# Optimization experiments

Measured on AMD Instinct MI355X. Metric: run time of the kernel, lower is better.

## Reference

```python
import jax, jax.numpy as jnp
import numpy as np

B, F, T, EPT, S, E, H, LVL = 16384, 512, 4, 2, 2, 256, 128, 2

def _ple_level(xs_task, x_sh, w_task, b_task, w_sh, b_sh, w_gate, b_gate, w_gsh=None, b_gsh=None):
    # xs_task: [T,B,I] per-task inputs; x_sh: [B,I] shared input
    task_out = jax.nn.relu(jnp.einsum('tbi,teio->tbeo', xs_task, w_task) + b_task[:, None])  # [T,B,EPT,E]
    sh_out = jax.nn.relu(jnp.einsum('bi,sio->bso', x_sh, w_sh) + b_sh)                       # [B,S,E]
    t = task_out.shape[0]
    experts = jnp.concatenate([task_out, jnp.broadcast_to(sh_out[None], (t,) + sh_out.shape)], axis=2)  # [T,B,EPT+S,E]
    gate = jax.nn.softmax(jnp.einsum('tbi,tig->tbg', xs_task, w_gate) + b_gate[:, None], axis=-1)
    task_next = jnp.einsum('tbg,tbge->tbe', gate, experts)  # [T,B,E]
    sh_next = None
    if w_gsh is not None:
        # all experts ordered task0_exp0, task0_exp1, task1_exp0, ..., then shared
        bsz = x_sh.shape[0]
        all_exp = jnp.concatenate([jnp.transpose(task_out, (1, 0, 2, 3)).reshape(bsz, -1, task_out.shape[-1]), sh_out], axis=1)
        gsh = jax.nn.softmax(x_sh @ w_gsh + b_gsh, axis=-1)
        sh_next = jnp.einsum('bg,bge->be', gsh, all_exp)
    return task_next, sh_next

def setup_inputs() -> dict:
    key = jax.random.key(0)
    ks = jax.random.split(key, 16)
    sc = 0.02
    d = {
        'x': jax.random.normal(ks[0], (B, F), jnp.float32),
        # level 0 (in_dim=F, has shared gate)
        'w_task0': jax.random.normal(ks[1], (T, EPT, F, E), jnp.float32) * sc,
        'b_task0': jnp.zeros((T, EPT, E), jnp.float32),
        'w_sh0': jax.random.normal(ks[2], (S, F, E), jnp.float32) * sc,
        'b_sh0': jnp.zeros((S, E), jnp.float32),
        'w_gate0': jax.random.normal(ks[3], (T, F, EPT + S), jnp.float32) * sc,
        'b_gate0': jnp.zeros((T, EPT + S), jnp.float32),
        'w_gsh0': jax.random.normal(ks[4], (F, T * EPT + S), jnp.float32) * sc,
        'b_gsh0': jnp.zeros((T * EPT + S,), jnp.float32),
        # level 1 (last; in_dim=E, no shared gate)
        'w_task1': jax.random.normal(ks[5], (T, EPT, E, E), jnp.float32) * sc,
        'b_task1': jnp.zeros((T, EPT, E), jnp.float32),
        'w_sh1': jax.random.normal(ks[6], (S, E, E), jnp.float32) * sc,
        'b_sh1': jnp.zeros((S, E), jnp.float32),
        'w_gate1': jax.random.normal(ks[7], (T, E, EPT + S), jnp.float32) * sc,
        'b_gate1': jnp.zeros((T, EPT + S), jnp.float32),
        # towers
        'w_tw': jax.random.normal(ks[8], (T, E, H), jnp.float32) * sc,
        'b_tw': jnp.zeros((T, H), jnp.float32),
        'w_out': jax.random.normal(ks[9], (T, H, 2), jnp.float32) * sc,
        'b_out': jnp.zeros((T, 2), jnp.float32),
    }
    return d

def reference(x, w_task0, b_task0, w_sh0, b_sh0, w_gate0, b_gate0, w_gsh0, b_gsh0,
              w_task1, b_task1, w_sh1, b_sh1, w_gate1, b_gate1,
              w_tw, b_tw, w_out, b_out):
    xs_task = jnp.broadcast_to(x[None], (T,) + x.shape)  # all tasks see same input at level 0
    t1, sh1 = _ple_level(xs_task, x, w_task0, b_task0, w_sh0, b_sh0, w_gate0, b_gate0, w_gsh0, b_gsh0)
    t2, _ = _ple_level(t1, sh1, w_task1, b_task1, w_sh1, b_sh1, w_gate1, b_gate1)
    h = jax.nn.relu(jnp.einsum('tbe,teh->tbh', t2, w_tw) + b_tw[:, None])
    logits = jnp.einsum('tbh,tho->tbo', h, w_out) + b_out[:, None]
    p = jax.nn.softmax(logits, axis=-1)
    return jnp.clip(p, 1e-15, 1.0 - 1e-15)  # [T,B,2]
```

## Files before the change

kernel.cpp:

```cpp
#include <hip/hip_runtime.h>

typedef unsigned short u16;
typedef __bf16 bf16x8 __attribute__((ext_vector_type(8)));
typedef float f32x4 __attribute__((ext_vector_type(4)));
typedef u16 u16x8 __attribute__((ext_vector_type(8)));

#define B_ 16384

__device__ __forceinline__ u16 f2b(float f){
  unsigned u = __builtin_bit_cast(unsigned, f);
  u = (u + 0x7FFFu + ((u >> 16) & 1u)) >> 16;
  return (u16)u;
}
__device__ __forceinline__ float b2f(u16 v){
  return __builtin_bit_cast(float, ((unsigned)v) << 16);
}
__device__ __forceinline__ void ld8(const u16* __restrict__ p, float* f){
  u16x8 v = *(const u16x8*)p;
  #pragma unroll
  for (int j = 0; j < 8; ++j) f[j] = b2f(v[j]);
}
__device__ __forceinline__ void st8(u16* __restrict__ p, const float* f){
  u16x8 v;
  #pragma unroll
  for (int j = 0; j < 8; ++j) v[j] = f2b(f[j]);
  *(u16x8*)p = v;
}

__device__ __forceinline__ void gload16(const u16* g, u16* lds){
  __builtin_amdgcn_global_load_lds(
      (const __attribute__((address_space(1))) unsigned int*)g,
      (__attribute__((address_space(3))) unsigned int*)lds, 16, 0, 0);
}

__device__ __forceinline__ void gemm_core4(const u16* __restrict__ A,
                                           const u16* __restrict__ Wt,
                                           int K, int m0, int n0, int nt,
                                           u16* sm, f32x4 acc[4][4])
{
  const int tid  = threadIdx.x;
  const int lane = tid & 63;
  const int wave = tid >> 6;
  const int wm   = ((tid >> 7) & 1) * 64;
  const int wn   = ((tid >> 6) & 1) * 64;

  f32x4 zero = {0.f, 0.f, 0.f, 0.f};
  #pragma unroll
  for (int mi = 0; mi < 4; ++mi)
    #pragma unroll
    for (int ni = 0; ni < 4; ++ni) acc[mi][ni] = zero;

  const int srow  = lane >> 3;
  const int gslot = (lane & 7) ^ srow;
  const u16* gsrc[8];
  int gdst[8];
  #pragma unroll
  for (int i = 0; i < 8; ++i) {
    int c = wave * 8 + i;
    if (c < 16) {
      gsrc[i] = A + (size_t)(m0 + c * 8 + srow) * K + gslot * 8;
      gdst[i] = c * 512;
    } else {
      gsrc[i] = Wt + (size_t)(n0 + (c - 16) * 8 + srow) * K + gslot * 8;
      gdst[i] = 8192 + (c - 16) * 512;
    }
  }

  int aoff[2][4], boff[2][4];
  #pragma unroll
  for (int kk = 0; kk < 2; ++kk) {
    #pragma unroll
    for (int m = 0; m < 4; ++m) {
      int r = wm + m * 16 + (lane & 15);
      aoff[kk][m] = r * 64 + (((kk * 4 + (lane >> 4)) ^ (r & 7)) * 8);
    }
    #pragma unroll
    for (int n = 0; n < 4; ++n) {
      int r = wn + n * 16 + (lane & 15);
      boff[kk][n] = 8192 + r * 64 + (((kk * 4 + (lane >> 4)) ^ (r & 7)) * 8);
    }
  }

  #pragma unroll
  for (int i = 0; i < 8; ++i) gload16(gsrc[i], sm + gdst[i]);
  asm volatile("s_waitcnt vmcnt(0)" ::: "memory");
  __builtin_amdgcn_s_barrier();

  for (int j = 0; j < nt; ++j) {
    if (j + 1 < nt) {
      u16* base = sm + ((j + 1) & 1) * 16384;
      #pragma unroll
      for (int i = 0; i < 8; ++i) gload16(gsrc[i] + (size_t)(j + 1) * 64, base + gdst[i]);
    }
    const u16* sa = sm + (j & 1) * 16384;
    #pragma unroll
    for (int kk = 0; kk < 2; ++kk) {
      bf16x8 av[4], bv[4];
      #pragma unroll
      for (int m = 0; m < 4; ++m) av[m] = *(const bf16x8*)(sa + aoff[kk][m]);
      #pragma unroll
      for (int n = 0; n < 4; ++n) bv[n] = *(const bf16x8*)(sa + boff[kk][n]);
      #pragma unroll
      for (int m = 0; m < 4; ++m)
        #pragma unroll
        for (int n = 0; n < 4; ++n)
          acc[m][n] = __builtin_amdgcn_mfma_f32_16x16x32_bf16(av[m], bv[n], acc[m][n], 0, 0, 0);
    }
    if (j + 1 < nt) {
      asm volatile("s_waitcnt vmcnt(0)" ::: "memory");
      __builtin_amdgcn_s_barrier();
    }
  }
}


__global__ __launch_bounds__(256) void k_gemm0(const u16* __restrict__ xb,
    const u16* __restrict__ Wt0, const float* __restrict__ bias0,
    u16* __restrict__ E0, float* __restrict__ G0L)
{
  __shared__ __align__(16) u16 sm[32768];
  f32x4 acc[4][4];
  const int bid = blockIdx.x;
  const int swz = (bid & 7) * 336 + (bid >> 3);
  const int m0 = (swz / 21) * 128, n0 = (swz % 21) * 128;
  gemm_core4(xb, Wt0, 512, m0, n0, 8, sm, acc);
  const int lane = threadIdx.x & 63;
  const int wm = ((threadIdx.x >> 7) & 1) * 64, wn = ((threadIdx.x >> 6) & 1) * 64;
  #pragma unroll
  for (int mi = 0; mi < 4; ++mi)
    #pragma unroll
    for (int ni = 0; ni < 4; ++ni) {
      int gcol = n0 + wn + ni * 16 + (lane & 15);
      float bias = bias0[gcol];
      #pragma unroll
      for (int r = 0; r < 4; ++r) {
        int grow = m0 + wm + mi * 16 + ((lane >> 4) << 2) + r;
        float v = acc[mi][ni][r] + bias;
        if (gcol < 2560)      E0[(size_t)grow * 2560 + gcol] = f2b(fmaxf(v, 0.f));
        else if (gcol < 2586) G0L[(size_t)grow * 26 + (gcol - 2560)] = v;
      }
    }
}

__global__ __launch_bounds__(256) void k_mix0(const u16* __restrict__ E0,
    const float* __restrict__ G0L, u16* __restrict__ T1SH)
{
  const int b = blockIdx.x * 8 + (threadIdx.x >> 5);
  const int e0 = (threadIdx.x & 31) * 8;
  const float* gl = G0L + (size_t)b * 26;
  float g[4][4];
  #pragma unroll
  for (int t = 0; t < 4; ++t) {
    float l0 = gl[t*4+0], l1 = gl[t*4+1], l2 = gl[t*4+2], l3 = gl[t*4+3];
    float m = fmaxf(fmaxf(l0, l1), fmaxf(l2, l3));
    float e0e = expf(l0-m), e1 = expf(l1-m), e2 = expf(l2-m), e3 = expf(l3-m);
    float inv = 1.f / (e0e + e1 + e2 + e3);
    g[t][0] = e0e*inv; g[t][1] = e1*inv; g[t][2] = e2*inv; g[t][3] = e3*inv;
  }
  float gs[10];
  {
    float m = gl[16];
    #pragma unroll
    for (int j = 1; j < 10; ++j) m = fmaxf(m, gl[16 + j]);
    float s = 0.f;
    #pragma unroll
    for (int j = 0; j < 10; ++j) { gs[j] = expf(gl[16 + j] - m); s += gs[j]; }
    float inv = 1.f / s;
    #pragma unroll
    for (int j = 0; j < 10; ++j) gs[j] *= inv;
  }
  const u16* row = E0 + (size_t)b * 2560;
  float sh0[8], sh1[8], shacc[8];
  ld8(row + 2048 + e0, sh0);
  ld8(row + 2304 + e0, sh1);
  #pragma unroll
  for (int j = 0; j < 8; ++j) shacc[j] = gs[8]*sh0[j] + gs[9]*sh1[j];
  #pragma unroll
  for (int t = 0; t < 4; ++t) {
    float te0[8], te1[8], v[8];
    ld8(row + (t*2+0)*256 + e0, te0);
    ld8(row + (t*2+1)*256 + e0, te1);
    #pragma unroll
    for (int j = 0; j < 8; ++j) {
      v[j] = g[t][0]*te0[j] + g[t][1]*te1[j] + g[t][2]*sh0[j] + g[t][3]*sh1[j];
      shacc[j] += gs[t*2+0]*te0[j] + gs[t*2+1]*te1[j];
    }
    st8(T1SH + ((size_t)t * B_ + b) * 256 + e0, v);
  }
  st8(T1SH + ((size_t)4 * B_ + b) * 256 + e0, shacc);
}

__global__ __launch_bounds__(256) void k_gemm1(const u16* __restrict__ T1SH,
    const u16* __restrict__ Wt1, const float* __restrict__ bias1,
    u16* __restrict__ E1, float* __restrict__ G1L, u16* __restrict__ SH1E)
{
  const int z = blockIdx.z;
  const int m0 = blockIdx.x * 128, n0 = blockIdx.y * 128;
  if (z == 4 && n0 >= 512) return;
  __shared__ __align__(16) u16 sm[32768];
  f32x4 acc[4][4];
  gemm_core4(T1SH + (size_t)z * B_ * 256, Wt1 + (size_t)z * 640 * 256, 256, m0, n0, 4, sm, acc);
  const int lane = threadIdx.x & 63;
  const int wm = ((threadIdx.x >> 7) & 1) * 64, wn = ((threadIdx.x >> 6) & 1) * 64;
  const float* bias = bias1 + z * 640;
  #pragma unroll
  for (int mi = 0; mi < 4; ++mi)
    #pragma unroll
    for (int ni = 0; ni < 4; ++ni) {
      int gcol = n0 + wn + ni * 16 + (lane & 15);
      float bv = bias[gcol];
      #pragma unroll
      for (int r = 0; r < 4; ++r) {
        int grow = m0 + wm + mi * 16 + ((lane >> 4) << 2) + r;
        float v = acc[mi][ni][r] + bv;
        if (z < 4) {
          if (gcol < 512)      E1[((size_t)z * B_ + grow) * 512 + gcol] = f2b(fmaxf(v, 0.f));
          else if (gcol < 516) G1L[((size_t)z * B_ + grow) * 4 + (gcol - 512)] = v;
        } else {
          if (gcol < 512)      SH1E[(size_t)grow * 512 + gcol] = f2b(fmaxf(v, 0.f));
        }
      }
    }
}

__global__ __launch_bounds__(256) void k_mix1(const u16* __restrict__ E1,
    const float* __restrict__ G1L, const u16* __restrict__ SH1E, u16* __restrict__ T2)
{
  const int b = blockIdx.x * 8 + (threadIdx.x >> 5);
  const int e0 = (threadIdx.x & 31) * 8;
  float sh0[8], sh1[8];
  ld8(SH1E + (size_t)b * 512 + e0, sh0);
  ld8(SH1E + (size_t)b * 512 + 256 + e0, sh1);
  #pragma unroll
  for (int t = 0; t < 4; ++t) {
    const float* gl = G1L + ((size_t)t * B_ + b) * 4;
    float l0 = gl[0], l1 = gl[1], l2 = gl[2], l3 = gl[3];
    float m = fmaxf(fmaxf(l0, l1), fmaxf(l2, l3));
    float x0 = expf(l0-m), x1 = expf(l1-m), x2 = expf(l2-m), x3 = expf(l3-m);
    float inv = 1.f / (x0 + x1 + x2 + x3);
    float g0 = x0*inv, g1 = x1*inv, g2 = x2*inv, g3 = x3*inv;
    float te0[8], te1[8], v[8];
    ld8(E1 + ((size_t)t * B_ + b) * 512 + e0, te0);
    ld8(E1 + ((size_t)t * B_ + b) * 512 + 256 + e0, te1);
    #pragma unroll
    for (int j = 0; j < 8; ++j)
      v[j] = g0*te0[j] + g1*te1[j] + g2*sh0[j] + g3*sh1[j];
    st8(T2 + ((size_t)t * B_ + b) * 256 + e0, v);
  }
}

__global__ __launch_bounds__(256) void k_tower(const u16* __restrict__ T2,
    const u16* __restrict__ Wtw, const float* __restrict__ b_tw,
    const float* __restrict__ w_out, const float* __restrict__ b_out,
    float* __restrict__ out)
{
  __shared__ __align__(16) u16 sm[32768];
  __shared__ float part[2][128][2];
  f32x4 acc[4][4];
  const int z = blockIdx.z;
  const int m0 = blockIdx.x * 128;
  gemm_core4(T2 + (size_t)z * B_ * 256, Wtw + (size_t)z * 128 * 256, 256, m0, 0, 4, sm, acc);
  const int lane = threadIdx.x & 63;
  const int wm = ((threadIdx.x >> 7) & 1) * 64, wn = ((threadIdx.x >> 6) & 1) * 64;
  #pragma unroll
  for (int mi = 0; mi < 4; ++mi) {
    #pragma unroll
    for (int r = 0; r < 4; ++r) {
      float p0 = 0.f, p1 = 0.f;
      #pragma unroll
      for (int ni = 0; ni < 4; ++ni) {
        int col = wn + ni * 16 + (lane & 15);
        float h = fmaxf(acc[mi][ni][r] + b_tw[z * 128 + col], 0.f);
        p0 += h * w_out[(z * 128 + col) * 2 + 0];
        p1 += h * w_out[(z * 128 + col) * 2 + 1];
      }
      #pragma unroll
      for (int off = 1; off < 16; off <<= 1) {
        p0 += __shfl_xor(p0, off);
        p1 += __shfl_xor(p1, off);
      }
      if ((lane & 15) == 0) {
        int rowl = wm + mi * 16 + ((lane >> 4) << 2) + r;
        part[wn >> 6][rowl][0] = p0;
        part[wn >> 6][rowl][1] = p1;
      }
    }
  }
  __syncthreads();
  if (threadIdx.x < 128) {
    int rowl = threadIdx.x;
    float l0 = part[0][rowl][0] + part[1][rowl][0] + b_out[z * 2 + 0];
    float l1 = part[0][rowl][1] + part[1][rowl][1] + b_out[z * 2 + 1];
    float mx = fmaxf(l0, l1);
    float e0 = expf(l0 - mx), e1 = expf(l1 - mx);
    float inv = 1.f / (e0 + e1);
    float p0 = fminf(fmaxf(e0 * inv, 1e-15f), 1.0f);
    float p1 = fminf(fmaxf(e1 * inv, 1e-15f), 1.0f);
    size_t o = ((size_t)z * B_ + m0 + rowl) * 2;
    out[o] = p0; out[o + 1] = p1;
  }
}

__global__ void k_prep(const float* __restrict__ x,
    const float* __restrict__ w_task0, const float* __restrict__ b_task0,
    const float* __restrict__ w_sh0,   const float* __restrict__ b_sh0,
    const float* __restrict__ w_gate0, const float* __restrict__ b_gate0,
    const float* __restrict__ w_gsh0,  const float* __restrict__ b_gsh0,
    const float* __restrict__ w_task1, const float* __restrict__ b_task1,
    const float* __restrict__ w_sh1,   const float* __restrict__ b_sh1,
    const float* __restrict__ w_gate1, const float* __restrict__ b_gate1,
    const float* __restrict__ w_tw,
    u16* __restrict__ xb, u16* __restrict__ Wt0, float* __restrict__ bias0,
    u16* __restrict__ Wt1, float* __restrict__ bias1, u16* __restrict__ Wtw)
{
  size_t i = (size_t)blockIdx.x * 256 + threadIdx.x;
  const size_t S_X8  = (size_t)16384 * 512 / 8;
  const size_t S_WT0 = (size_t)2688 * 512;
  const size_t S_B0  = 2688;
  const size_t S_WT1 = (size_t)5 * 640 * 256;
  const size_t S_B1  = 5 * 640;
  const size_t S_WTW = (size_t)4 * 128 * 256;

  if (i < S_X8) {
    size_t o = i * 8;
    float4 a = *(const float4*)(x + o);
    float4 b = *(const float4*)(x + o + 4);
    u16x8 v;
    v[0] = f2b(a.x); v[1] = f2b(a.y); v[2] = f2b(a.z); v[3] = f2b(a.w);
    v[4] = f2b(b.x); v[5] = f2b(b.y); v[6] = f2b(b.z); v[7] = f2b(b.w);
    *(u16x8*)(xb + o) = v;
    return;
  }
  i -= S_X8;
  if (i < S_WT0) {
    int c = (int)(i / 512), f = (int)(i % 512);
    float v = 0.f;
    if (c < 2048)      { int te = c >> 8, o = c & 255; v = w_task0[((size_t)te * 512 + f) * 256 + o]; }
    else if (c < 2560) { int s = (c - 2048) >> 8, o = c & 255; v = w_sh0[((size_t)s * 512 + f) * 256 + o]; }
    else if (c < 2576) { int q = c - 2560; int t = q >> 2, gg = q & 3; v = w_gate0[((size_t)t * 512 + f) * 4 + gg]; }
    else if (c < 2586) { int j = c - 2576; v = w_gsh0[(size_t)f * 10 + j]; }
    Wt0[i] = f2b(v);
    return;
  }
  i -= S_WT0;
  if (i < S_B0) {
    int c = (int)i; float v = 0.f;
    if (c < 2048)      { int te = c >> 8, o = c & 255; v = b_task0[te * 256 + o]; }
    else if (c < 2560) { int s = (c - 2048) >> 8, o = c & 255; v = b_sh0[s * 256 + o]; }
    else if (c < 2576) { v = b_gate0[c - 2560]; }
    else if (c < 2586) { v = b_gsh0[c - 2576]; }
    bias0[c] = v;
    return;
  }
  i -= S_B0;
  if (i < S_WT1) {
    int z = (int)(i / (640 * 256)); int rem = (int)(i % (640 * 256));
    int c = rem / 256, f = rem % 256;
    float v = 0.f;
    if (z < 4) {
      if (c < 512)      { int ee = c >> 8, o = c & 255; v = w_task1[(((size_t)(z * 2 + ee)) * 256 + f) * 256 + o]; }
      else if (c < 516) { int gg = c - 512; v = w_gate1[((size_t)z * 256 + f) * 4 + gg]; }
    } else {
      if (c < 512)      { int s = c >> 8, o = c & 255; v = w_sh1[((size_t)s * 256 + f) * 256 + o]; }
    }
    Wt1[i] = f2b(v);
    return;
  }
  i -= S_WT1;
  if (i < S_B1) {
    int z = (int)(i / 640); int c = (int)(i % 640);
    float v = 0.f;
    if (z < 4) {
      if (c < 512)      { int ee = c >> 8, o = c & 255; v = b_task1[(z * 2 + ee) * 256 + o]; }
      else if (c < 516) { v = b_gate1[z * 4 + (c - 512)]; }
    } else {
      if (c < 512)      { int s = c >> 8, o = c & 255; v = b_sh1[s * 256 + o]; }
    }
    bias1[(size_t)z * 640 + c] = v;
    return;
  }
  i -= S_B1;
  if (i < S_WTW) {
    int z = (int)(i / (128 * 256)); int rem = (int)(i % (128 * 256));
    int h = rem / 256, f = rem % 256;
    Wtw[i] = f2b(w_tw[((size_t)z * 256 + f) * 128 + h]);
    return;
  }
}

extern "C" void kernel_launch(void* const* d_in, const int* in_sizes, int n_in,
                              void* d_out, int out_size, void* d_ws, size_t ws_size,
                              hipStream_t stream)
{
  (void)in_sizes; (void)n_in; (void)out_size; (void)ws_size;
  const float* x       = (const float*)d_in[0];
  const float* w_task0 = (const float*)d_in[1];
  const float* b_task0 = (const float*)d_in[2];
  const float* w_sh0   = (const float*)d_in[3];
  const float* b_sh0   = (const float*)d_in[4];
  const float* w_gate0 = (const float*)d_in[5];
  const float* b_gate0 = (const float*)d_in[6];
  const float* w_gsh0  = (const float*)d_in[7];
  const float* b_gsh0  = (const float*)d_in[8];
  const float* w_task1 = (const float*)d_in[9];
  const float* b_task1 = (const float*)d_in[10];
  const float* w_sh1   = (const float*)d_in[11];
  const float* b_sh1   = (const float*)d_in[12];
  const float* w_gate1 = (const float*)d_in[13];
  const float* b_gate1 = (const float*)d_in[14];
  const float* w_tw    = (const float*)d_in[15];
  const float* b_tw    = (const float*)d_in[16];
  const float* w_out   = (const float*)d_in[17];
  const float* b_out   = (const float*)d_in[18];
  float* out = (float*)d_out;

  char* ws = (char*)d_ws;
  u16*   XB    = (u16*)  (ws + 0);
  u16*   WT0   = (u16*)  (ws + 16777216);
  float* BIAS0 = (float*)(ws + 19529728);
  u16*   WT1   = (u16*)  (ws + 19540480);
  float* BIAS1 = (float*)(ws + 21178880);
  u16*   WTW   = (u16*)  (ws + 21191680);
  u16*   E0    = (u16*)  (ws + 21453824);
  float* G0L   = (float*)(ws + 105339904);
  u16*   T1SH  = (u16*)  (ws + 107043840);
  u16*   E1    = (u16*)  (ws + 148986880);
  float* G1L   = (float*)(ws + 216095744);
  u16*   SH1E  = (u16*)  (ws + 217144320);
  u16*   T2    = (u16*)  (ws + 21453824);

  k_prep<<<13207, 256, 0, stream>>>(x, w_task0, b_task0, w_sh0, b_sh0, w_gate0, b_gate0,
      w_gsh0, b_gsh0, w_task1, b_task1, w_sh1, b_sh1, w_gate1, b_gate1, w_tw,
      XB, WT0, BIAS0, WT1, BIAS1, WTW);
  k_gemm0<<<2688, 256, 0, stream>>>(XB, WT0, BIAS0, E0, G0L);
  k_mix0<<<2048, 256, 0, stream>>>(E0, G0L, T1SH);
  k_gemm1<<<dim3(128, 5, 5), 256, 0, stream>>>(T1SH, WT1, BIAS1, E1, G1L, SH1E);
  k_mix1<<<2048, 256, 0, stream>>>(E1, G1L, SH1E, T2);
  k_tower<<<dim3(128, 1, 4), 256, 0, stream>>>(T2, WTW, b_tw, w_out, b_out, out);
}
```

Before: 211.7 us.

## Fuse level-0 expert GEMM with gate mixing, split gate logits into separate kernel

Replaces the level-0 GEMM plus separate mixing kernel with a small gate kernel that computes the softmaxed gates per row, and a fused GEMM that computes expert outputs in 64-row tiles and applies the gated mixing in its epilogue. Each block walks the task-expert pairs and then the shared experts through a three-slot LDS pipeline. The large bf16 E0 intermediate is never written to or read back from memory. In exchange there is an extra launch, only 512 blocks, and a read-modify-write of T1SH for the shared contributions, which adds an extra bf16 rounding step.

Result: slower. 447.5 us (+111.4%).

```diff
diff --git a/kernel.cpp b/kernel.cpp
--- a/kernel.cpp
+++ b/kernel.cpp
@@ -31,6 +31,221 @@
   __builtin_amdgcn_global_load_lds(
       (const __attribute__((address_space(1))) unsigned int*)g,
       (__attribute__((address_space(3))) unsigned int*)lds, 16, 0, 0);
+}
+
+__global__ __launch_bounds__(256) void k_gate0(const u16* __restrict__ xb,
+    const u16* __restrict__ Wt0, const float* __restrict__ bias0,
+    float* __restrict__ G0S)
+{
+  const int lane = threadIdx.x & 63, wave = threadIdx.x >> 6;
+  const int rbase = blockIdx.x * 64 + wave * 16;
+  u16x8 w[26];
+  #pragma unroll
+  for (int g = 0; g < 26; ++g)
+    w[g] = *(const u16x8*)(Wt0 + (size_t)(2560 + g) * 512 + lane * 8);
+  float bias[26];
+  #pragma unroll
+  for (int g = 0; g < 26; ++g) bias[g] = bias0[2560 + g];
+
+  for (int it = 0; it < 16; ++it) {
+    int row = rbase + it;
+    float f[8]; ld8(xb + (size_t)row * 512 + lane * 8, f);
+    float lg[26];
+    #pragma unroll
+    for (int g = 0; g < 26; ++g) {
+      float p = 0.f;
+      #pragma unroll
+      for (int j = 0; j < 8; ++j) p += f[j] * b2f(w[g][j]);
+      #pragma unroll
+      for (int off = 1; off < 64; off <<= 1) p += __shfl_xor(p, off);
+      lg[g] = p + bias[g];
+    }
+    float tg[16];
+    #pragma unroll
+    for (int t = 0; t < 4; ++t) {
+      float m = fmaxf(fmaxf(lg[4*t], lg[4*t+1]), fmaxf(lg[4*t+2], lg[4*t+3]));
+      float e0 = expf(lg[4*t]-m), e1 = expf(lg[4*t+1]-m);
+      float e2 = expf(lg[4*t+2]-m), e3 = expf(lg[4*t+3]-m);
+      float inv = 1.f / (e0+e1+e2+e3);
+      tg[4*t] = e0*inv; tg[4*t+1] = e1*inv; tg[4*t+2] = e2*inv; tg[4*t+3] = e3*inv;
+    }
+    float sg[10];
+    {
+      float m = lg[16];
+      #pragma unroll
+      for (int j = 1; j < 10; ++j) m = fmaxf(m, lg[16+j]);
+      float ssum = 0.f;
+      #pragma unroll
+      for (int j = 0; j < 10; ++j) { sg[j] = expf(lg[16+j]-m); ssum += sg[j]; }
+      float inv = 1.f / ssum;
+      #pragma unroll
+      for (int j = 0; j < 10; ++j) sg[j] *= inv;
+    }
+    float* orow = G0S + (size_t)row * 32;
+    #pragma unroll
+    for (int g = 0; g < 16; ++g) if (lane == g) orow[g] = tg[g];
+    #pragma unroll
+    for (int j = 0; j < 10; ++j) if (lane == 16 + j) orow[16 + j] = sg[j];
+  }
+}
+
+__global__ __launch_bounds__(256, 2) void k_fused0(const u16* __restrict__ xb,
+    const u16* __restrict__ Wt0, const float* __restrict__ bias0,
+    const float* __restrict__ G0S, u16* __restrict__ T1SH)
+{
+  __shared__ __align__(16) u16 sm[30720];
+  const int tid = threadIdx.x, lane = tid & 63, wave = tid >> 6;
+  const int bid = blockIdx.x;
+  const int swz = (bid & 7) * 64 + (bid >> 3);
+  const int m0 = (swz >> 1) * 64, np = swz & 1;
+
+  const int srow = lane >> 2;
+  const int sig  = ((lane & 3) - (lane >> 3)) & 3;
+  size_t aOff[5]; int bOff[5]; int ldst[5]; bool isA[5];
+  #pragma unroll
+  for (int i = 0; i < 5; ++i) {
+    int c = wave * 5 + i;
+    if (c < 4) {
+      isA[i] = true;
+      aOff[i] = (size_t)(m0 + c * 16 + srow) * 512 + sig * 8;
+      bOff[i] = 0;
+      ldst[i] = c * 512;
+    } else {
+      isA[i] = false;
+      int rho = (c - 4) * 16 + srow;
+      aOff[i] = 0;
+      bOff[i] = (np * 128 + rho + (rho >= 128 ? 128 : 0)) * 512 + sig * 8;
+      ldst[i] = 2048 + (c - 4) * 512;
+    }
+  }
+
+  int aoff[4], boff[2];
+  #pragma unroll
+  for (int m = 0; m < 4; ++m) {
+    int r = m * 16 + (lane & 15);
+    aoff[m] = r * 32 + ((((lane >> 4) + (r >> 1)) & 3) * 8);
+  }
+  #pragma unroll
+  for (int n = 0; n < 2; ++n) {
+    int br = wave * 32 + n * 16 + (lane & 15);
+    boff[n] = 2048 + br * 32 + ((((lane >> 4) + (br >> 1)) & 3) * 8);
+  }
+
+  f32x4 zero = {0.f,0.f,0.f,0.f};
+  f32x4 acc_lo[4][2], acc_hi[4][2], shacc[4][2];
+  #pragma unroll
+  for (int m = 0; m < 4; ++m)
+    #pragma unroll
+    for (int n = 0; n < 2; ++n) { acc_lo[m][n] = zero; acc_hi[m][n] = zero; shacc[m][n] = zero; }
+
+  #define STAGE(S, SLOT) do {                                                  \
+    int js_ = ((S) & 15) * 32;                                                 \
+    int ps_ = (S) >> 4;                                                        \
+    int bb_ = (ps_ < 4) ? ps_ * 262144 : 1048576;                              \
+    u16* sl_ = sm + (SLOT) * 10240;                                            \
+    _Pragma("unroll")                                                          \
+    for (int i_ = 0; i_ < 5; ++i_) {                                           \
+      const u16* src_ = isA[i_] ? (xb + aOff[i_] + js_)                        \
+                                : (Wt0 + bOff[i_] + bb_ + js_);                \
+      gload16(src_, sl_ + ldst[i_]);                                           \
+    }                                                                          \
+  } while (0)
+
+  STAGE(0, 0);
+  STAGE(1, 1);
+  asm volatile("s_waitcnt vmcnt(5)" ::: "memory");
+  __builtin_amdgcn_s_barrier();
+
+  const int elbase = wave * 32 + (lane & 15);
+  int s = 0, cs = 0;
+  for (int p = 0; p < 5; ++p) {
+    for (int j = 0; j < 16; ++j, ++s) {
+      if (s + 2 < 80) {
+        int ns = cs + 2; ns = (ns >= 3) ? ns - 3 : ns;
+        STAGE(s + 2, ns);
+      }
+      const u16* sa = sm + cs * 10240;
+      bf16x8 av[4], bl[2], bh[2];
+      #pragma unroll
+      for (int m = 0; m < 4; ++m) av[m] = *(const bf16x8*)(sa + aoff[m]);
+      #pragma unroll
+      for (int n = 0; n < 2; ++n) {
+        bl[n] = *(const bf16x8*)(sa + boff[n]);
+        bh[n] = *(const bf16x8*)(sa + boff[n] + 4096);
+      }
+      #pragma unroll
+      for (int m = 0; m < 4; ++m)
+        #pragma unroll
+        for (int n = 0; n < 2; ++n) {
+          acc_lo[m][n] = __builtin_amdgcn_mfma_f32_16x16x32_bf16(av[m], bl[n], acc_lo[m][n], 0, 0, 0);
+          acc_hi[m][n] = __builtin_amdgcn_mfma_f32_16x16x32_bf16(av[m], bh[n], acc_hi[m][n], 0, 0, 0);
+        }
+      if (s + 2 < 80)      asm volatile("s_waitcnt vmcnt(5)" ::: "memory");
+      else if (s + 1 < 80) asm volatile("s_waitcnt vmcnt(0)" ::: "memory");
+      if (s + 1 < 80) __builtin_amdgcn_s_barrier();
+      cs = (cs == 2) ? 0 : cs + 1;
+    }
+    if (p < 4) {
+      int bbase = p * 512 + np * 128;
+      float bl0 = bias0[bbase + elbase],       bl1 = bias0[bbase + elbase + 16];
+      float bh0 = bias0[bbase + 256 + elbase], bh1 = bias0[bbase + 256 + elbase + 16];
+      #pragma unroll
+      for (int mi = 0; mi < 4; ++mi)
+        #pragma unroll
+        for (int q = 0; q < 4; ++q) {
+          int r = m0 + mi * 16 + ((lane >> 4) << 2) + q;
+          const float* gp = G0S + (size_t)r * 32;
+          float4 g  = *(const float4*)(gp + p * 4);
+          float2 gsv = *(const float2*)(gp + 16 + p * 2);
+          #pragma unroll
+          for (int n = 0; n < 2; ++n) {
+            float lo = fmaxf(acc_lo[mi][n][q] + (n ? bl1 : bl0), 0.f);
+            float hi = fmaxf(acc_hi[mi][n][q] + (n ? bh1 : bh0), 0.f);
+            int col = np * 128 + elbase + n * 16;
+            T1SH[((size_t)p * B_ + r) * 256 + col] = f2b(g.x * lo + g.y * hi);
+            shacc[mi][n][q] += gsv.x * lo + gsv.y * hi;
+          }
+        }
+      #pragma unroll
+      for (int m = 0; m < 4; ++m)
+        #pragma unroll
+        for (int n = 0; n < 2; ++n) { acc_lo[m][n] = zero; acc_hi[m][n] = zero; }
+    } else {
+      asm volatile("s_waitcnt vmcnt(0)" ::: "memory");
+      int bbase = 2048 + np * 128;
+      float bl0 = bias0[bbase + elbase],       bl1 = bias0[bbase + elbase + 16];
+      float bh0 = bias0[bbase + 256 + elbase], bh1 = bias0[bbase + 256 + elbase + 16];
+      #pragma unroll
+      for (int mi = 0; mi < 4; ++mi)
+        #pragma unroll
+        for (int q = 0; q < 4; ++q) {
+          int r = m0 + mi * 16 + ((lane >> 4) << 2) + q;
+          const float* gp = G0S + (size_t)r * 32;
+          float4 g0 = *(const float4*)(gp + 0);
+          float4 g1 = *(const float4*)(gp + 4);
+          float4 g2 = *(const float4*)(gp + 8);
+          float4 g3 = *(const float4*)(gp + 12);
+          float gs8 = gp[24], gs9 = gp[25];
+          #pragma unroll
+          for (int n = 0; n < 2; ++n) {
+            float shlo = fmaxf(acc_lo[mi][n][q] + (n ? bl1 : bl0), 0.f);
+            float shhi = fmaxf(acc_hi[mi][n][q] + (n ? bh1 : bh0), 0.f);
+            int col = np * 128 + elbase + n * 16;
+            size_t i0 = ((size_t)0 * B_ + r) * 256 + col;
+            size_t i1 = ((size_t)1 * B_ + r) * 256 + col;
+            size_t i2 = ((size_t)2 * B_ + r) * 256 + col;
+            size_t i3 = ((size_t)3 * B_ + r) * 256 + col;
+            T1SH[i0] = f2b(b2f(T1SH[i0]) + g0.z * shlo + g0.w * shhi);
+            T1SH[i1] = f2b(b2f(T1SH[i1]) + g1.z * shlo + g1.w * shhi);
+            T1SH[i2] = f2b(b2f(T1SH[i2]) + g2.z * shlo + g2.w * shhi);
+            T1SH[i3] = f2b(b2f(T1SH[i3]) + g3.z * shlo + g3.w * shhi);
+            float sv = shacc[mi][n][q] + gs8 * shlo + gs9 * shhi;
+            T1SH[((size_t)4 * B_ + r) * 256 + col] = f2b(sv);
+          }
+        }
+    }
+  }
+  #undef STAGE
 }
 
 __device__ __forceinline__ void gemm_core4(const u16* __restrict__ A,
@@ -111,83 +326,6 @@
       __builtin_amdgcn_s_barrier();
     }
   }
-}
-
-
-__global__ __launch_bounds__(256) void k_gemm0(const u16* __restrict__ xb,
-    const u16* __restrict__ Wt0, const float* __restrict__ bias0,
-    u16* __restrict__ E0, float* __restrict__ G0L)
-{
-  __shared__ __align__(16) u16 sm[32768];
-  f32x4 acc[4][4];
-  const int bid = blockIdx.x;
-  const int swz = (bid & 7) * 336 + (bid >> 3);
-  const int m0 = (swz / 21) * 128, n0 = (swz % 21) * 128;
-  gemm_core4(xb, Wt0, 512, m0, n0, 8, sm, acc);
-  const int lane = threadIdx.x & 63;
-  const int wm = ((threadIdx.x >> 7) & 1) * 64, wn = ((threadIdx.x >> 6) & 1) * 64;
-  #pragma unroll
-  for (int mi = 0; mi < 4; ++mi)
-    #pragma unroll
-    for (int ni = 0; ni < 4; ++ni) {
-      int gcol = n0 + wn + ni * 16 + (lane & 15);
-      float bias = bias0[gcol];
-      #pragma unroll
-      for (int r = 0; r < 4; ++r) {
-        int grow = m0 + wm + mi * 16 + ((lane >> 4) << 2) + r;
-        float v = acc[mi][ni][r] + bias;
-        if (gcol < 2560)      E0[(size_t)grow * 2560 + gcol] = f2b(fmaxf(v, 0.f));
-        else if (gcol < 2586) G0L[(size_t)grow * 26 + (gcol - 2560)] = v;
-      }
-    }
-}
-
-__global__ __launch_bounds__(256) void k_mix0(const u16* __restrict__ E0,
-    const float* __restrict__ G0L, u16* __restrict__ T1SH)
-{
-  const int b = blockIdx.x * 8 + (threadIdx.x >> 5);
-  const int e0 = (threadIdx.x & 31) * 8;
-  const float* gl = G0L + (size_t)b * 26;
-  float g[4][4];
-  #pragma unroll
-  for (int t = 0; t < 4; ++t) {
-    float l0 = gl[t*4+0], l1 = gl[t*4+1], l2 = gl[t*4+2], l3 = gl[t*4+3];
-    float m = fmaxf(fmaxf(l0, l1), fmaxf(l2, l3));
-    float e0e = expf(l0-m), e1 = expf(l1-m), e2 = expf(l2-m), e3 = expf(l3-m);
-    float inv = 1.f / (e0e + e1 + e2 + e3);
-    g[t][0] = e0e*inv; g[t][1] = e1*inv; g[t][2] = e2*inv; g[t][3] = e3*inv;
-  }
-  float gs[10];
-  {
-    float m = gl[16];
-    #pragma unroll
-    for (int j = 1; j < 10; ++j) m = fmaxf(m, gl[16 + j]);
-    float s = 0.f;
-    #pragma unroll
-    for (int j = 0; j < 10; ++j) { gs[j] = expf(gl[16 + j] - m); s += gs[j]; }
-    float inv = 1.f / s;
-    #pragma unroll
-    for (int j = 0; j < 10; ++j) gs[j] *= inv;
-  }
-  const u16* row = E0 + (size_t)b * 2560;
-  float sh0[8], sh1[8], shacc[8];
-  ld8(row + 2048 + e0, sh0);
-  ld8(row + 2304 + e0, sh1);
-  #pragma unroll
-  for (int j = 0; j < 8; ++j) shacc[j] = gs[8]*sh0[j] + gs[9]*sh1[j];
-  #pragma unroll
-  for (int t = 0; t < 4; ++t) {
-    float te0[8], te1[8], v[8];
-    ld8(row + (t*2+0)*256 + e0, te0);
-    ld8(row + (t*2+1)*256 + e0, te1);
-    #pragma unroll
-    for (int j = 0; j < 8; ++j) {
-      v[j] = g[t][0]*te0[j] + g[t][1]*te1[j] + g[t][2]*sh0[j] + g[t][3]*sh1[j];
-      shacc[j] += gs[t*2+0]*te0[j] + gs[t*2+1]*te1[j];
-    }
-    st8(T1SH + ((size_t)t * B_ + b) * 256 + e0, v);
-  }
-  st8(T1SH + ((size_t)4 * B_ + b) * 256 + e0, shacc);
 }
 
 __global__ __launch_bounds__(256) void k_gemm1(const u16* __restrict__ T1SH,
@@ -421,19 +559,18 @@
   u16*   WT1   = (u16*)  (ws + 19540480);
   float* BIAS1 = (float*)(ws + 21178880);
   u16*   WTW   = (u16*)  (ws + 21191680);
-  u16*   E0    = (u16*)  (ws + 21453824);
-  float* G0L   = (float*)(ws + 105339904);
+  float* G0S   = (float*)(ws + 21453824);
+  u16*   T2    = (u16*)  (ws + 23550976);
   u16*   T1SH  = (u16*)  (ws + 107043840);
   u16*   E1    = (u16*)  (ws + 148986880);
   float* G1L   = (float*)(ws + 216095744);
   u16*   SH1E  = (u16*)  (ws + 217144320);
-  u16*   T2    = (u16*)  (ws + 21453824);
 
   k_prep<<<13207, 256, 0, stream>>>(x, w_task0, b_task0, w_sh0, b_sh0, w_gate0, b_gate0,
       w_gsh0, b_gsh0, w_task1, b_task1, w_sh1, b_sh1, w_gate1, b_gate1, w_tw,
       XB, WT0, BIAS0, WT1, BIAS1, WTW);
-  k_gemm0<<<2688, 256, 0, stream>>>(XB, WT0, BIAS0, E0, G0L);
-  k_mix0<<<2048, 256, 0, stream>>>(E0, G0L, T1SH);
+  k_gate0<<<256, 256, 0, stream>>>(XB, WT0, BIAS0, G0S);
+  k_fused0<<<512, 256, 0, stream>>>(XB, WT0, BIAS0, G0S, T1SH);
   k_gemm1<<<dim3(128, 5, 5), 256, 0, stream>>>(T1SH, WT1, BIAS1, E1, G1L, SH1E);
   k_mix1<<<2048, 256, 0, stream>>>(E1, G1L, SH1E, T2);
   k_tower<<<dim3(128, 1, 4), 256, 0, stream>>>(T2, WTW, b_tw, w_out, b_out, out);
```

## Use 256x256 GEMM tiles and split level-1 gate into separate kernel

Applied to the files above, without the earlier changes.

Replaces the 128x128, 256-thread GEMM core with a 256x256, 512-thread core that uses XOR-swizzled LDS, double buffering and MFMA priority hints, for both level GEMMs. Level 1's four gate columns are moved out of the GEMM into a new small k_gate1 kernel that computes the softmax gates directly. This lets GEMM1 use exact 512-column panels with no wasted 640-column padding, and mix1 reads precomputed gates. The larger tiles increase register and LDS pressure, lowering occupancy, and k_gate1 adds one launch plus a reread of T1SH.

Result: slower. 223.1 us (+5.4%).

```diff
diff --git a/kernel.cpp b/kernel.cpp
--- a/kernel.cpp
+++ b/kernel.cpp
@@ -4,6 +4,7 @@
 typedef __bf16 bf16x8 __attribute__((ext_vector_type(8)));
 typedef float f32x4 __attribute__((ext_vector_type(4)));
 typedef u16 u16x8 __attribute__((ext_vector_type(8)));
+typedef u16 u16x4 __attribute__((ext_vector_type(4)));
 
 #define B_ 16384
 
@@ -31,6 +32,254 @@
   __builtin_amdgcn_global_load_lds(
       (const __attribute__((address_space(1))) unsigned int*)g,
       (__attribute__((address_space(3))) unsigned int*)lds, 16, 0, 0);
+}
+
+__device__ __forceinline__ void core256(const u16* __restrict__ A,
+                                        const u16* __restrict__ Wt,
+                                        int K, int m0, int n0, int nt,
+                                        u16* sm, f32x4 acc[8][4])
+{
+  const int tid = threadIdx.x, lane = tid & 63;
+  const int wm = (tid >> 8) * 128;
+  const int wn = ((tid >> 6) & 3) * 64;
+
+  #pragma unroll
+  for (int m = 0; m < 8; ++m)
+    #pragma unroll
+    for (int n = 0; n < 4; ++n) acc[m][n] = (f32x4){0.f, 0.f, 0.f, 0.f};
+
+  const int srow  = tid >> 3;
+  const int sslot = (tid & 7) ^ (srow & 7);
+  const u16* psrc[8];
+  int pdst[8];
+  const int wbase = (tid >> 6) * 512;
+  #pragma unroll
+  for (int g = 0; g < 4; ++g) {
+    psrc[g]     = A  + (size_t)(m0 + g * 64 + srow) * K + sslot * 8;
+    pdst[g]     = g * 4096 + wbase;
+    psrc[g + 4] = Wt + (size_t)(n0 + g * 64 + srow) * K + sslot * 8;
+    pdst[g + 4] = 16384 + g * 4096 + wbase;
+  }
+
+  int abase[2], bbase[2];
+  #pragma unroll
+  for (int kk = 0; kk < 2; ++kk) {
+    int phys = (kk * 4 + (lane >> 4)) ^ (lane & 7);
+    abase[kk] = (wm + (lane & 15)) * 64 + phys * 8;
+    bbase[kk] = 16384 + (wn + (lane & 15)) * 64 + phys * 8;
+  }
+
+  #pragma unroll
+  for (int g = 0; g < 8; ++g) gload16(psrc[g], sm + pdst[g]);
+  asm volatile("s_waitcnt vmcnt(0)" ::: "memory");
+  __builtin_amdgcn_s_barrier();
+
+  for (int t = 0; t < nt; ++t) {
+    if (t + 1 < nt) {
+      u16* sl = sm + ((t + 1) & 1) * 32768;
+      #pragma unroll
+      for (int g = 0; g < 8; ++g) gload16(psrc[g] + (size_t)(t + 1) * 64, sl + pdst[g]);
+    }
+    const u16* s = sm + (t & 1) * 32768;
+    #pragma unroll
+    for (int kk = 0; kk < 2; ++kk) {
+      bf16x8 bv[4];
+      #pragma unroll
+      for (int n = 0; n < 4; ++n) bv[n] = *(const bf16x8*)(s + bbase[kk] + n * 1024);
+      #pragma unroll
+      for (int mh = 0; mh < 2; ++mh) {
+        bf16x8 av[4];
+        #pragma unroll
+        for (int m = 0; m < 4; ++m) av[m] = *(const bf16x8*)(s + abase[kk] + (mh * 4 + m) * 1024);
+        __builtin_amdgcn_s_setprio(1);
+        #pragma unroll
+        for (int m = 0; m < 4; ++m)
+          #pragma unroll
+          for (int n = 0; n < 4; ++n)
+            acc[mh*4+m][n] = __builtin_amdgcn_mfma_f32_16x16x32_bf16(av[m], bv[n], acc[mh*4+m][n], 0, 0, 0);
+        __builtin_amdgcn_s_setprio(0);
+      }
+    }
+    if (t + 1 < nt) {
+      asm volatile("s_waitcnt vmcnt(0)" ::: "memory");
+      __builtin_amdgcn_s_barrier();
+    }
+  }
+}
+
+
+__global__ __launch_bounds__(512) void k_gemm0(const u16* __restrict__ xb,
+    const u16* __restrict__ Wt0, const float* __restrict__ bias0,
+    u16* __restrict__ E0, float* __restrict__ G0L)
+{
+  __shared__ __align__(16) u16 sm[65536];
+  f32x4 acc[8][4];
+  const int bid = blockIdx.x;
+  const int swz = (bid & 7) * 88 + (bid >> 3);
+  const int m0 = (swz / 11) * 256, n0 = (swz % 11) * 256;
+  core256(xb, Wt0, 512, m0, n0, 8, sm, acc);
+  const int lane = threadIdx.x & 63;
+  const int wm = (threadIdx.x >> 8) * 128, wn = ((threadIdx.x >> 6) & 3) * 64;
+  #pragma unroll
+  for (int mi = 0; mi < 8; ++mi)
+    #pragma unroll
+    for (int ni = 0; ni < 4; ++ni) {
+      int gcol = n0 + wn + ni * 16 + (lane & 15);
+      float bias = bias0[gcol];
+      #pragma unroll
+      for (int q = 0; q < 4; ++q) {
+        int grow = m0 + wm + mi * 16 + ((lane >> 4) << 2) + q;
+        float v = acc[mi][ni][q] + bias;
+        if (gcol < 2560)      E0[(size_t)grow * 2560 + gcol] = f2b(fmaxf(v, 0.f));
+        else if (gcol < 2586) G0L[(size_t)grow * 26 + (gcol - 2560)] = v;
+      }
+    }
+}
+
+__global__ __launch_bounds__(256) void k_mix0(const u16* __restrict__ E0,
+    const float* __restrict__ G0L, u16* __restrict__ T1SH)
+{
+  const int b = blockIdx.x * 8 + (threadIdx.x >> 5);
+  const int e0 = (threadIdx.x & 31) * 8;
+  const float* gl = G0L + (size_t)b * 26;
+  float g[4][4];
+  #pragma unroll
+  for (int t = 0; t < 4; ++t) {
+    float l0 = gl[t*4+0], l1 = gl[t*4+1], l2 = gl[t*4+2], l3 = gl[t*4+3];
+    float m = fmaxf(fmaxf(l0, l1), fmaxf(l2, l3));
+    float e0e = expf(l0-m), e1 = expf(l1-m), e2 = expf(l2-m), e3 = expf(l3-m);
+    float inv = 1.f / (e0e + e1 + e2 + e3);
+    g[t][0] = e0e*inv; g[t][1] = e1*inv; g[t][2] = e2*inv; g[t][3] = e3*inv;
+  }
+  float gs[10];
+  {
+    float m = gl[16];
+    #pragma unroll
+    for (int j = 1; j < 10; ++j) m = fmaxf(m, gl[16 + j]);
+    float s = 0.f;
+    #pragma unroll
+    for (int j = 0; j < 10; ++j) { gs[j] = expf(gl[16 + j] - m); s += gs[j]; }
+    float inv = 1.f / s;
+    #pragma unroll
+    for (int j = 0; j < 10; ++j) gs[j] *= inv;
+  }
+  const u16* row = E0 + (size_t)b * 2560;
+  float sh0[8], sh1[8], shacc[8];
+  ld8(row + 2048 + e0, sh0);
+  ld8(row + 2304 + e0, sh1);
+  #pragma unroll
+  for (int j = 0; j < 8; ++j) shacc[j] = gs[8]*sh0[j] + gs[9]*sh1[j];
+  #pragma unroll
+  for (int t = 0; t < 4; ++t) {
+    float te0[8], te1[8], v[8];
+    ld8(row + (t*2+0)*256 + e0, te0);
+    ld8(row + (t*2+1)*256 + e0, te1);
+    #pragma unroll
+    for (int j = 0; j < 8; ++j) {
+      v[j] = g[t][0]*te0[j] + g[t][1]*te1[j] + g[t][2]*sh0[j] + g[t][3]*sh1[j];
+      shacc[j] += gs[t*2+0]*te0[j] + gs[t*2+1]*te1[j];
+    }
+    st8(T1SH + ((size_t)t * B_ + b) * 256 + e0, v);
+  }
+  st8(T1SH + ((size_t)4 * B_ + b) * 256 + e0, shacc);
+}
+
+__global__ __launch_bounds__(256) void k_gate1(const u16* __restrict__ T1SH,
+    const float* __restrict__ w_gate1, const float* __restrict__ b_gate1,
+    float* __restrict__ G1S)
+{
+  const int lane = threadIdx.x & 63, wave = threadIdx.x >> 6;
+  const int rbase = blockIdx.x * 64 + wave * 16;
+  float w[16][4];
+  #pragma unroll
+  for (int zg = 0; zg < 16; ++zg) {
+    int z = zg >> 2, gg = zg & 3;
+    #pragma unroll
+    for (int j = 0; j < 4; ++j)
+      w[zg][j] = w_gate1[((size_t)z * 256 + lane * 4 + j) * 4 + gg];
+  }
+  for (int it = 0; it < 16; ++it) {
+    int row = rbase + it;
+    float lg[16];
+    #pragma unroll
+    for (int z = 0; z < 4; ++z) {
+      u16x4 tv = *(const u16x4*)(T1SH + ((size_t)z * B_ + row) * 256 + lane * 4);
+      float f0 = b2f(tv[0]), f1 = b2f(tv[1]), f2 = b2f(tv[2]), f3 = b2f(tv[3]);
+      #pragma unroll
+      for (int gg = 0; gg < 4; ++gg) {
+        float p = f0*w[z*4+gg][0] + f1*w[z*4+gg][1] + f2*w[z*4+gg][2] + f3*w[z*4+gg][3];
+        #pragma unroll
+        for (int off = 1; off < 64; off <<= 1) p += __shfl_xor(p, off);
+        lg[z*4+gg] = p + b_gate1[z*4+gg];
+      }
+    }
+    float gt[16];
+    #pragma unroll
+    for (int z = 0; z < 4; ++z) {
+      float l0=lg[z*4],l1=lg[z*4+1],l2=lg[z*4+2],l3=lg[z*4+3];
+      float m = fmaxf(fmaxf(l0,l1),fmaxf(l2,l3));
+      float e0=expf(l0-m),e1=expf(l1-m),e2=expf(l2-m),e3=expf(l3-m);
+      float inv = 1.f/(e0+e1+e2+e3);
+      gt[z*4]=e0*inv; gt[z*4+1]=e1*inv; gt[z*4+2]=e2*inv; gt[z*4+3]=e3*inv;
+    }
+    float* orow = G1S + (size_t)row * 16;
+    #pragma unroll
+    for (int gg = 0; gg < 16; ++gg) if (lane == gg) orow[gg] = gt[gg];
+  }
+}
+
+__global__ __launch_bounds__(512) void k_gemm1(const u16* __restrict__ T1SH,
+    const u16* __restrict__ Wt1, const float* __restrict__ bias1,
+    u16* __restrict__ E1, u16* __restrict__ SH1E)
+{
+  __shared__ __align__(16) u16 sm[65536];
+  f32x4 acc[8][4];
+  const int bid = blockIdx.x;
+  const int swz = (bid & 7) * 80 + (bid >> 3);
+  const int mi_ = swz / 10, pan = swz % 10;
+  const int z  = (pan < 8) ? (pan >> 1) : 4;
+  const int n0 = (pan < 8) ? (pan & 1) * 256 : (pan - 8) * 256;
+  const int m0 = mi_ * 256;
+  core256(T1SH + (size_t)z * B_ * 256, Wt1 + (size_t)z * 512 * 256, 256, m0, n0, 4, sm, acc);
+  const int lane = threadIdx.x & 63;
+  const int wm = (threadIdx.x >> 8) * 128, wn = ((threadIdx.x >> 6) & 3) * 64;
+  const float* bias = bias1 + z * 512;
+  #pragma unroll
+  for (int mi = 0; mi < 8; ++mi)
+    #pragma unroll
+    for (int ni = 0; ni < 4; ++ni) {
+      int gcol = n0 + wn + ni * 16 + (lane & 15);
+      float bv = bias[gcol];
+      #pragma unroll
+      for (int q = 0; q < 4; ++q) {
+        int grow = m0 + wm + mi * 16 + ((lane >> 4) << 2) + q;
+        float v = fmaxf(acc[mi][ni][q] + bv, 0.f);
+        if (z < 4) E1[((size_t)z * B_ + grow) * 512 + gcol] = f2b(v);
+        else       SH1E[(size_t)grow * 512 + gcol] = f2b(v);
+      }
+    }
+}
+
+__global__ __launch_bounds__(256) void k_mix1(const u16* __restrict__ E1,
+    const float* __restrict__ G1S, const u16* __restrict__ SH1E, u16* __restrict__ T2)
+{
+  const int b = blockIdx.x * 8 + (threadIdx.x >> 5);
+  const int e0 = (threadIdx.x & 31) * 8;
+  float sh0[8], sh1[8];
+  ld8(SH1E + (size_t)b * 512 + e0, sh0);
+  ld8(SH1E + (size_t)b * 512 + 256 + e0, sh1);
+  const float* gr = G1S + (size_t)b * 16;
+  #pragma unroll
+  for (int t = 0; t < 4; ++t) {
+    float g0 = gr[t*4+0], g1 = gr[t*4+1], g2 = gr[t*4+2], g3 = gr[t*4+3];
+    float te0[8], te1[8], v[8];
+    ld8(E1 + ((size_t)t * B_ + b) * 512 + e0, te0);
+    ld8(E1 + ((size_t)t * B_ + b) * 512 + 256 + e0, te1);
+    #pragma unroll
+    for (int j = 0; j < 8; ++j)
+      v[j] = g0*te0[j] + g1*te1[j] + g2*sh0[j] + g3*sh1[j];
+    st8(T2 + ((size_t)t * B_ + b) * 256 + e0, v);
+  }
 }
 
 __device__ __forceinline__ void gemm_core4(const u16* __restrict__ A,
@@ -110,142 +359,6 @@
       asm volatile("s_waitcnt vmcnt(0)" ::: "memory");
       __builtin_amdgcn_s_barrier();
     }
-  }
-}
-
-
-__global__ __launch_bounds__(256) void k_gemm0(const u16* __restrict__ xb,
-    const u16* __restrict__ Wt0, const float* __restrict__ bias0,
-    u16* __restrict__ E0, float* __restrict__ G0L)
-{
-  __shared__ __align__(16) u16 sm[32768];
-  f32x4 acc[4][4];
-  const int bid = blockIdx.x;
-  const int swz = (bid & 7) * 336 + (bid >> 3);
-  const int m0 = (swz / 21) * 128, n0 = (swz % 21) * 128;
-  gemm_core4(xb, Wt0, 512, m0, n0, 8, sm, acc);
-  const int lane = threadIdx.x & 63;
-  const int wm = ((threadIdx.x >> 7) & 1) * 64, wn = ((threadIdx.x >> 6) & 1) * 64;
-  #pragma unroll
-  for (int mi = 0; mi < 4; ++mi)
-    #pragma unroll
-    for (int ni = 0; ni < 4; ++ni) {
-      int gcol = n0 + wn + ni * 16 + (lane & 15);
-      float bias = bias0[gcol];
-      #pragma unroll
-      for (int r = 0; r < 4; ++r) {
-        int grow = m0 + wm + mi * 16 + ((lane >> 4) << 2) + r;
-        float v = acc[mi][ni][r] + bias;
-        if (gcol < 2560)      E0[(size_t)grow * 2560 + gcol] = f2b(fmaxf(v, 0.f));
-        else if (gcol < 2586) G0L[(size_t)grow * 26 + (gcol - 2560)] = v;
-      }
-    }
-}
-
-__global__ __launch_bounds__(256) void k_mix0(const u16* __restrict__ E0,
-    const float* __restrict__ G0L, u16* __restrict__ T1SH)
-{
-  const int b = blockIdx.x * 8 + (threadIdx.x >> 5);
-  const int e0 = (threadIdx.x & 31) * 8;
-  const float* gl = G0L + (size_t)b * 26;
-  float g[4][4];
-  #pragma unroll
-  for (int t = 0; t < 4; ++t) {
-    float l0 = gl[t*4+0], l1 = gl[t*4+1], l2 = gl[t*4+2], l3 = gl[t*4+3];
-    float m = fmaxf(fmaxf(l0, l1), fmaxf(l2, l3));
-    float e0e = expf(l0-m), e1 = expf(l1-m), e2 = expf(l2-m), e3 = expf(l3-m);
-    float inv = 1.f / (e0e + e1 + e2 + e3);
-    g[t][0] = e0e*inv; g[t][1] = e1*inv; g[t][2] = e2*inv; g[t][3] = e3*inv;
-  }
-  float gs[10];
-  {
-    float m = gl[16];
-    #pragma unroll
-    for (int j = 1; j < 10; ++j) m = fmaxf(m, gl[16 + j]);
-    float s = 0.f;
-    #pragma unroll
-    for (int j = 0; j < 10; ++j) { gs[j] = expf(gl[16 + j] - m); s += gs[j]; }
-    float inv = 1.f / s;
-    #pragma unroll
-    for (int j = 0; j < 10; ++j) gs[j] *= inv;
-  }
-  const u16* row = E0 + (size_t)b * 2560;
-  float sh0[8], sh1[8], shacc[8];
-  ld8(row + 2048 + e0, sh0);
-  ld8(row + 2304 + e0, sh1);
-  #pragma unroll
-  for (int j = 0; j < 8; ++j) shacc[j] = gs[8]*sh0[j] + gs[9]*sh1[j];
-  #pragma unroll
-  for (int t = 0; t < 4; ++t) {
-    float te0[8], te1[8], v[8];
-    ld8(row + (t*2+0)*256 + e0, te0);
-    ld8(row + (t*2+1)*256 + e0, te1);
-    #pragma unroll
-    for (int j = 0; j < 8; ++j) {
-      v[j] = g[t][0]*te0[j] + g[t][1]*te1[j] + g[t][2]*sh0[j] + g[t][3]*sh1[j];
-      shacc[j] += gs[t*2+0]*te0[j] + gs[t*2+1]*te1[j];
-    }
-    st8(T1SH + ((size_t)t * B_ + b) * 256 + e0, v);
-  }
-  st8(T1SH + ((size_t)4 * B_ + b) * 256 + e0, shacc);
-}
-
-__global__ __launch_bounds__(256) void k_gemm1(const u16* __restrict__ T1SH,
-    const u16* __restrict__ Wt1, const float* __restrict__ bias1,
-    u16* __restrict__ E1, float* __restrict__ G1L, u16* __restrict__ SH1E)
-{
-  const int z = blockIdx.z;
-  const int m0 = blockIdx.x * 128, n0 = blockIdx.y * 128;
-  if (z == 4 && n0 >= 512) return;
-  __shared__ __align__(16) u16 sm[32768];
-  f32x4 acc[4][4];
-  gemm_core4(T1SH + (size_t)z * B_ * 256, Wt1 + (size_t)z * 640 * 256, 256, m0, n0, 4, sm, acc);
-  const int lane = threadIdx.x & 63;
-  const int wm = ((threadIdx.x >> 7) & 1) * 64, wn = ((threadIdx.x >> 6) & 1) * 64;
-  const float* bias = bias1 + z * 640;
-  #pragma unroll
-  for (int mi = 0; mi < 4; ++mi)
-    #pragma unroll
-    for (int ni = 0; ni < 4; ++ni) {
-      int gcol = n0 + wn + ni * 16 + (lane & 15);
-      float bv = bias[gcol];
-      #pragma unroll
-      for (int r = 0; r < 4; ++r) {
-        int grow = m0 + wm + mi * 16 + ((lane >> 4) << 2) + r;
-        float v = acc[mi][ni][r] + bv;
-        if (z < 4) {
-          if (gcol < 512)      E1[((size_t)z * B_ + grow) * 512 + gcol] = f2b(fmaxf(v, 0.f));
-          else if (gcol < 516) G1L[((size_t)z * B_ + grow) * 4 + (gcol - 512)] = v;
-        } else {
-          if (gcol < 512)      SH1E[(size_t)grow * 512 + gcol] = f2b(fmaxf(v, 0.f));
-        }
-      }
-    }
-}
-
-__global__ __launch_bounds__(256) void k_mix1(const u16* __restrict__ E1,
-    const float* __restrict__ G1L, const u16* __restrict__ SH1E, u16* __restrict__ T2)
-{
-  const int b = blockIdx.x * 8 + (threadIdx.x >> 5);
-  const int e0 = (threadIdx.x & 31) * 8;
-  float sh0[8], sh1[8];
-  ld8(SH1E + (size_t)b * 512 + e0, sh0);
-  ld8(SH1E + (size_t)b * 512 + 256 + e0, sh1);
-  #pragma unroll
-  for (int t = 0; t < 4; ++t) {
-    const float* gl = G1L + ((size_t)t * B_ + b) * 4;
-    float l0 = gl[0], l1 = gl[1], l2 = gl[2], l3 = gl[3];
-    float m = fmaxf(fmaxf(l0, l1), fmaxf(l2, l3));
-    float x0 = expf(l0-m), x1 = expf(l1-m), x2 = expf(l2-m), x3 = expf(l3-m);
-    float inv = 1.f / (x0 + x1 + x2 + x3);
-    float g0 = x0*inv, g1 = x1*inv, g2 = x2*inv, g3 = x3*inv;
-    float te0[8], te1[8], v[8];
-    ld8(E1 + ((size_t)t * B_ + b) * 512 + e0, te0);
-    ld8(E1 + ((size_t)t * B_ + b) * 512 + 256 + e0, te1);
-    #pragma unroll
-    for (int j = 0; j < 8; ++j)
-      v[j] = g0*te0[j] + g1*te1[j] + g2*sh0[j] + g3*sh1[j];
-    st8(T2 + ((size_t)t * B_ + b) * 256 + e0, v);
   }
 }
 
@@ -308,17 +421,16 @@
     const float* __restrict__ w_gsh0,  const float* __restrict__ b_gsh0,
     const float* __restrict__ w_task1, const float* __restrict__ b_task1,
     const float* __restrict__ w_sh1,   const float* __restrict__ b_sh1,
-    const float* __restrict__ w_gate1, const float* __restrict__ b_gate1,
     const float* __restrict__ w_tw,
     u16* __restrict__ xb, u16* __restrict__ Wt0, float* __restrict__ bias0,
     u16* __restrict__ Wt1, float* __restrict__ bias1, u16* __restrict__ Wtw)
 {
   size_t i = (size_t)blockIdx.x * 256 + threadIdx.x;
   const size_t S_X8  = (size_t)16384 * 512 / 8;
-  const size_t S_WT0 = (size_t)2688 * 512;
-  const size_t S_B0  = 2688;
-  const size_t S_WT1 = (size_t)5 * 640 * 256;
-  const size_t S_B1  = 5 * 640;
+  const size_t S_WT0 = (size_t)2816 * 512;
+  const size_t S_B0  = 2816;
+  const size_t S_WT1 = (size_t)5 * 512 * 256;
+  const size_t S_B1  = 5 * 512;
   const size_t S_WTW = (size_t)4 * 128 * 256;
 
   if (i < S_X8) {
@@ -354,29 +466,21 @@
   }
   i -= S_B0;
   if (i < S_WT1) {
-    int z = (int)(i / (640 * 256)); int rem = (int)(i % (640 * 256));
+    int z = (int)(i / (512 * 256)); int rem = (int)(i % (512 * 256));
     int c = rem / 256, f = rem % 256;
-    float v = 0.f;
-    if (z < 4) {
-      if (c < 512)      { int ee = c >> 8, o = c & 255; v = w_task1[(((size_t)(z * 2 + ee)) * 256 + f) * 256 + o]; }
-      else if (c < 516) { int gg = c - 512; v = w_gate1[((size_t)z * 256 + f) * 4 + gg]; }
-    } else {
-      if (c < 512)      { int s = c >> 8, o = c & 255; v = w_sh1[((size_t)s * 256 + f) * 256 + o]; }
-    }
+    float v;
+    if (z < 4) { int ee = c >> 8, o = c & 255; v = w_task1[(((size_t)(z * 2 + ee)) * 256 + f) * 256 + o]; }
+    else       { int s = c >> 8, o = c & 255; v = w_sh1[((size_t)s * 256 + f) * 256 + o]; }
     Wt1[i] = f2b(v);
     return;
   }
   i -= S_WT1;
   if (i < S_B1) {
-    int z = (int)(i / 640); int c = (int)(i % 640);
-    float v = 0.f;
-    if (z < 4) {
-      if (c < 512)      { int ee = c >> 8, o = c & 255; v = b_task1[(z * 2 + ee) * 256 + o]; }
-      else if (c < 516) { v = b_gate1[z * 4 + (c - 512)]; }
-    } else {
-      if (c < 512)      { int s = c >> 8, o = c & 255; v = b_sh1[s * 256 + o]; }
-    }
-    bias1[(size_t)z * 640 + c] = v;
+    int z = (int)(i / 512); int c = (int)(i % 512);
+    float v;
+    if (z < 4) { int ee = c >> 8, o = c & 255; v = b_task1[(z * 2 + ee) * 256 + o]; }
+    else       { int s = c >> 8, o = c & 255; v = b_sh1[s * 256 + o]; }
+    bias1[(size_t)z * 512 + c] = v;
     return;
   }
   i -= S_B1;
@@ -416,25 +520,26 @@
 
   char* ws = (char*)d_ws;
   u16*   XB    = (u16*)  (ws + 0);
+  u16*   SH1E  = (u16*)  (ws + 0);
   u16*   WT0   = (u16*)  (ws + 16777216);
-  float* BIAS0 = (float*)(ws + 19529728);
-  u16*   WT1   = (u16*)  (ws + 19540480);
-  float* BIAS1 = (float*)(ws + 21178880);
-  u16*   WTW   = (u16*)  (ws + 21191680);
-  u16*   E0    = (u16*)  (ws + 21453824);
-  float* G0L   = (float*)(ws + 105339904);
-  u16*   T1SH  = (u16*)  (ws + 107043840);
-  u16*   E1    = (u16*)  (ws + 148986880);
-  float* G1L   = (float*)(ws + 216095744);
-  u16*   SH1E  = (u16*)  (ws + 217144320);
-  u16*   T2    = (u16*)  (ws + 21453824);
-
-  k_prep<<<13207, 256, 0, stream>>>(x, w_task0, b_task0, w_sh0, b_sh0, w_gate0, b_gate0,
-      w_gsh0, b_gsh0, w_task1, b_task1, w_sh1, b_sh1, w_gate1, b_gate1, w_tw,
+  float* BIAS0 = (float*)(ws + 19660800);
+  u16*   WT1   = (u16*)  (ws + 19672064);
+  float* BIAS1 = (float*)(ws + 20982784);
+  u16*   WTW   = (u16*)  (ws + 20993024);
+  u16*   E0    = (u16*)  (ws + 21255168);
+  u16*   T2    = (u16*)  (ws + 21255168);
+  float* G0L   = (float*)(ws + 105141248);
+  u16*   T1SH  = (u16*)  (ws + 106845184);
+  u16*   E1    = (u16*)  (ws + 148788224);
+  float* G1S   = (float*)(ws + 215897088);
+
+  k_prep<<<12821, 256, 0, stream>>>(x, w_task0, b_task0, w_sh0, b_sh0, w_gate0, b_gate0,
+      w_gsh0, b_gsh0, w_task1, b_task1, w_sh1, b_sh1, w_tw,
       XB, WT0, BIAS0, WT1, BIAS1, WTW);
-  k_gemm0<<<2688, 256, 0, stream>>>(XB, WT0, BIAS0, E0, G0L);
+  k_gemm0<<<704, 512, 0, stream>>>(XB, WT0, BIAS0, E0, G0L);
   k_mix0<<<2048, 256, 0, stream>>>(E0, G0L, T1SH);
-  k_gemm1<<<dim3(128, 5, 5), 256, 0, stream>>>(T1SH, WT1, BIAS1, E1, G1L, SH1E);
-  k_mix1<<<2048, 256, 0, stream>>>(E1, G1L, SH1E, T2);
+  k_gate1<<<256, 256, 0, stream>>>(T1SH, w_gate1, b_gate1, G1S);
+  k_gemm1<<<640, 512, 0, stream>>>(T1SH, WT1, BIAS1, E1, SH1E);
+  k_mix1<<<2048, 256, 0, stream>>>(E1, G1S, SH1E, T2);
   k_tower<<<dim3(128, 1, 4), 256, 0, stream>>>(T2, WTW, b_tw, w_out, b_out, out);
 }
```
